# Kernel optimization log

Hardware: AMD Instinct MI355X
Metric: run time of the kernel (lower is better)

Reference implementation:

```python
import jax, jax.numpy as jnp
import numpy as np

L, B, N, W, H = 8, 8, 1024, 768, 12
C = W // H  # per-head channel dim = 64


def setup_inputs() -> dict:
    key = jax.random.key(0)
    ks = jax.random.split(key, 5)
    s = 0.02  # init scale for weights
    return {
        "x": jax.random.normal(ks[0], (B, N, W), jnp.float32),
        "Wqkv": jax.random.normal(ks[1], (L, W, 3 * W), jnp.float32) * s,
        "bqkv": jnp.zeros((L, 3 * W), jnp.float32),
        "Wo": jax.random.normal(ks[2], (L, W, W), jnp.float32) * s,
        "bo": jnp.zeros((L, W), jnp.float32),
        "Wfc": jax.random.normal(ks[3], (L, W, 4 * W), jnp.float32) * s,
        "bfc": jnp.zeros((L, 4 * W), jnp.float32),
        "Wpr": jax.random.normal(ks[4], (L, 4 * W, W), jnp.float32) * s,
        "bpr": jnp.zeros((L, W), jnp.float32),
        "g1": jnp.ones((L, W), jnp.float32),
        "b1": jnp.zeros((L, W), jnp.float32),
        "g2": jnp.ones((L, W), jnp.float32),
        "b2": jnp.zeros((L, W), jnp.float32),
    }


def _ln(x, g, b, eps=1e-5):
    m = jnp.mean(x, axis=-1, keepdims=True)
    v = jnp.var(x, axis=-1, keepdims=True)
    return (x - m) * jax.lax.rsqrt(v + eps) * g + b


def reference(x, Wqkv, bqkv, Wo, bo, Wfc, bfc, Wpr, bpr, g1, b1, g2, b2):
    scale = 1.0 / np.sqrt(np.sqrt(C))  # applied to BOTH q and k, as in source

    def block(h, p):
        wqkv, bq, wo, bo_, wfc, bf, wpr, bp, G1, B1, G2, B2 = p
        # --- attention ---
        y = _ln(h, G1, B1)
        qkv = y @ wqkv + bq                       # [B,N,3W]
        qkv = qkv.reshape(B, N, H, 3 * C)         # per-head interleaved q|k|v
        q, k, v = jnp.split(qkv, 3, axis=-1)      # each [B,N,H,C]
        w = jnp.einsum('bthc,bshc->bhts', q * scale, k * scale)
        w = jax.nn.softmax(w.astype(jnp.float32), axis=-1).astype(w.dtype)
        attn = jnp.einsum('bhts,bshc->bthc', w, v).reshape(B, N, W)
        h = h + attn @ wo + bo_
        # --- MLP (exact GELU, matching torch F.gelu default) ---
        y2 = _ln(h, G2, B2)
        h = h + jax.nn.gelu(y2 @ wfc + bf, approximate=False) @ wpr + bp
        return h, None

    out, _ = jax.lax.scan(block, x, (Wqkv, bqkv, Wo, bo, Wfc, bfc, Wpr, bpr, g1, b1, g2, b2))
    return out
```

## Files before the change

kernel.cpp:

```cpp
#include <hip/hip_runtime.h>
#include <hip/hip_bf16.h>
#include <cstdint>
#include <cstddef>


typedef __attribute__((ext_vector_type(8))) short bf16x8;
typedef __attribute__((ext_vector_type(4))) float f32x4;

#define MFMA16(a, b, c) __builtin_amdgcn_mfma_f32_16x16x32_bf16((a), (b), (c), 0, 0, 0)

__device__ __forceinline__ void gld_lds16(const void* g, void* l) {
    __builtin_amdgcn_global_load_lds((const __attribute__((address_space(1))) unsigned int*)g,
                                     (__attribute__((address_space(3))) unsigned int*)l,
                                     16, 0, 0);
}

__device__ __forceinline__ unsigned short f32_to_bf16_bits(float f) {
    unsigned u = __builtin_bit_cast(unsigned, f);
    u += 0x7fffu + ((u >> 16) & 1u);
    return (unsigned short)(u >> 16);
}

__device__ __forceinline__ unsigned pack_bf2(float a, float b) {
    return (unsigned)f32_to_bf16_bits(a) | ((unsigned)f32_to_bf16_bits(b) << 16);
}

__device__ __forceinline__ unsigned cvt_pk_bf16(float lo, float hi) {
    unsigned r;
    asm("v_cvt_pk_bf16_f32 %0, %1, %2" : "=v"(r) : "v"(lo), "v"(hi));
    return r;
}

template <bool RES, bool GELU, bool WF, bool WH>
__global__ __launch_bounds__(256) void gemm_bt(const __hip_bfloat16* __restrict__ A,
                                               const __hip_bfloat16* __restrict__ Bt,
                                               const float* __restrict__ bias,
                                               const float* __restrict__ res,
                                               float* __restrict__ outf,
                                               __hip_bfloat16* __restrict__ outh,
                                               int N, int K) {
    __shared__ __hip_bfloat16 lA0[128 * 32], lA1[128 * 32];
    __shared__ __hip_bfloat16 lB0[128 * 32], lB1[128 * 32];
    const int t = threadIdx.x;
    const int w = t >> 6, l = t & 63;
    const int lr = l & 15, lg = l >> 4;
    const int bid = blockIdx.x;
    const int xcd = bid & 7;
    const int local = bid >> 3;
    const int m0 = (xcd * 8 + (local & 7)) * 128;
    const int n0 = (local >> 3) * 128;
    const int wm = (w & 1) * 64, wn = (w >> 1) * 64;

    f32x4 acc[4][4];
#pragma unroll
    for (int i = 0; i < 4; i++)
#pragma unroll
        for (int j = 0; j < 4; j++) acc[i][j] = (f32x4){0.f, 0.f, 0.f, 0.f};

    for (int k0 = 0; k0 < K; k0 += 64) {
        __syncthreads();
#pragma unroll
        for (int i = 0; i < 2; i++) {
            int c = t + i * 256;
            int row = c >> 2, seg = c & 3;
            const size_t ab = (size_t)(m0 + row) * K + k0 + seg * 8;
            const size_t bb = (size_t)(n0 + row) * K + k0 + seg * 8;
            gld_lds16(&A[ab],       &lA0[c * 8]);
            gld_lds16(&A[ab + 32],  &lA1[c * 8]);
            gld_lds16(&Bt[bb],      &lB0[c * 8]);
            gld_lds16(&Bt[bb + 32], &lB1[c * 8]);
        }
        __syncthreads();
#pragma unroll
        for (int hh = 0; hh < 2; hh++) {
            const __hip_bfloat16* sA = hh ? lA1 : lA0;
            const __hip_bfloat16* sB = hh ? lB1 : lB0;
            bf16x8 af[4], bfr[4];
#pragma unroll
            for (int mt = 0; mt < 4; mt++)
                af[mt] = *(const bf16x8*)&sA[(wm + mt * 16 + lr) * 32 + lg * 8];
#pragma unroll
            for (int nt = 0; nt < 4; nt++)
                bfr[nt] = *(const bf16x8*)&sB[(wn + nt * 16 + lr) * 32 + lg * 8];
#pragma unroll
            for (int mt = 0; mt < 4; mt++)
#pragma unroll
                for (int nt = 0; nt < 4; nt++)
                    acc[mt][nt] = MFMA16(af[mt], bfr[nt], acc[mt][nt]);
        }
    }

#pragma unroll
    for (int nt = 0; nt < 4; nt++) {
        const int col = n0 + wn + nt * 16 + lr;
        const float bv = bias[col];
#pragma unroll
        for (int mt = 0; mt < 4; mt++) {
#pragma unroll
            for (int r = 0; r < 4; r++) {
                const int row = m0 + wm + mt * 16 + lg * 4 + r;
                const size_t idx = (size_t)row * N + col;
                float v = acc[mt][nt][r] + bv;
                if (RES) v += res[idx];
                if (GELU) v = 0.5f * v * (1.f + erff(v * 0.70710678118654752f));
                if (WF) outf[idx] = v;
                if (WH) outh[idx] = __float2bfloat16(v);
            }
        }
    }
}

__global__ __launch_bounds__(256) void ln_kernel(const float* __restrict__ h,
                                                 const float* __restrict__ g,
                                                 const float* __restrict__ b,
                                                 __hip_bfloat16* __restrict__ y) {
    const int t = threadIdx.x;
    const int w = t >> 6, l = t & 63;
    const int row = blockIdx.x * 4 + w;
    const float4* hr = (const float4*)(h + (size_t)row * 768);
    const float4* g4 = (const float4*)g;
    const float4* b4 = (const float4*)b;
    float4 x[3];
    float s = 0.f, q = 0.f;
#pragma unroll
    for (int j = 0; j < 3; j++) {
        x[j] = hr[l + j * 64];
        s += x[j].x + x[j].y + x[j].z + x[j].w;
        q += x[j].x * x[j].x + x[j].y * x[j].y + x[j].z * x[j].z + x[j].w * x[j].w;
    }
#pragma unroll
    for (int d = 1; d < 64; d <<= 1) {
        s += __shfl_xor(s, d);
        q += __shfl_xor(q, d);
    }
    const float mean = s * (1.f / 768.f);
    const float var = q * (1.f / 768.f) - mean * mean;
    const float rs = rsqrtf(var + 1e-5f);
    uint2* yr = (uint2*)(y + (size_t)row * 768);
#pragma unroll
    for (int j = 0; j < 3; j++) {
        const float4 gg = g4[l + j * 64], bb = b4[l + j * 64];
        float o0 = (x[j].x - mean) * rs * gg.x + bb.x;
        float o1 = (x[j].y - mean) * rs * gg.y + bb.y;
        float o2 = (x[j].z - mean) * rs * gg.z + bb.z;
        float o3 = (x[j].w - mean) * rs * gg.w + bb.w;
        yr[l + j * 64] = make_uint2(pack_bf2(o0, o1), pack_bf2(o2, o3));
    }
}

__global__ __launch_bounds__(256) void transpose_weights(const float* __restrict__ sq,
                                                         const float* __restrict__ so,
                                                         const float* __restrict__ sf,
                                                         const float* __restrict__ sp,
                                                         __hip_bfloat16* __restrict__ dq,
                                                         __hip_bfloat16* __restrict__ dO,
                                                         __hip_bfloat16* __restrict__ df,
                                                         __hip_bfloat16* __restrict__ dp) {
    const int bid = blockIdx.x;
    const float* src;
    __hip_bfloat16* dst;
    int K, N, tloc;
    if (bid < 1728)      { src = sq; dst = dq; K = 768;  N = 2304; tloc = bid; }
    else if (bid < 2304) { src = so; dst = dO; K = 768;  N = 768;  tloc = bid - 1728; }
    else if (bid < 4608) { src = sf; dst = df; K = 768;  N = 3072; tloc = bid - 2304; }
    else                 { src = sp; dst = dp; K = 3072; N = 768;  tloc = bid - 4608; }
    const int ktiles = K / 32;
    const int k0 = (tloc % ktiles) * 32;
    const int n0 = (tloc / ktiles) * 32;
    const int t = threadIdx.x;
    __shared__ float tile[32][33];
#pragma unroll
    for (int p = 0; p < 4; p++) {
        int rr = p * 8 + (t >> 5);
        tile[rr][t & 31] = src[(size_t)(k0 + rr) * N + n0 + (t & 31)];
    }
    __syncthreads();
#pragma unroll
    for (int p = 0; p < 4; p++) {
        int rr = p * 8 + (t >> 5);
        dst[(size_t)(n0 + rr) * K + k0 + (t & 31)] = __float2bfloat16(tile[t & 31][rr]);
    }
}

__global__ __launch_bounds__(256) void vt_transpose(const short* __restrict__ qkv,
                                                    short* __restrict__ vt) {
    const int bid = blockIdx.x;
    const int bh = bid >> 6, tau = bid & 63;
    const int b = bh / 12, h = bh % 12;
    const int ct = tau >> 5, nt = tau & 31;
    const int n0 = nt * 32, c0 = ct * 32;
    const int t = threadIdx.x;
    __shared__ short tile[32][33];
    const short* base = qkv + (size_t)(b * 1024 + n0) * 2304 + h * 192 + 128 + c0;
#pragma unroll
    for (int p = 0; p < 4; p++) {
        int rr = p * 8 + (t >> 5);
        tile[rr][t & 31] = base[(size_t)rr * 2304 + (t & 31)];
    }
    __syncthreads();
    short* ob = vt + (size_t)((b * 12 + h) * 64 + c0) * 1024 + n0;
#pragma unroll
    for (int p = 0; p < 4; p++) {
        int rr = p * 8 + (t >> 5);
        ob[(size_t)rr * 1024 + (t & 31)] = tile[t & 31][rr];
    }
}

__global__ __launch_bounds__(256) void attn_kernel(const short* __restrict__ qkv,
                                                   const short* __restrict__ vt,
                                                   short* __restrict__ attnout) {
    const int bid = blockIdx.x;
    const int xcd = bid & 7, j = bid >> 3;
    const int bh = xcd * 12 + (j >> 4);
    const int qt = j & 15;
    const int b = bh / 12, hh = bh % 12;
    const int t = threadIdx.x, w = t >> 6, l = t & 63;
    const int lr = l & 15, lg = l >> 4;
    const int x7 = lr & 7;
    __shared__ short lK[64 * 64];
    __shared__ short lV[64 * 64];
    __shared__ short lP[4][16 * 64];
    const int qw = qt * 64 + w * 16;

    bf16x8 bq[2];
#pragma unroll
    for (int ks = 0; ks < 2; ks++)
        bq[ks] = *(const bf16x8*)&qkv[(size_t)(b * 1024 + qw + lr) * 2304 + hh * 192 + ks * 32 + lg * 8];

    int col[2];
    col[0] = (lg ^ x7) * 8;
    col[1] = ((4 | lg) ^ x7) * 8;

    const int c0 = t, c1 = t + 256;
    const int r0 = c0 >> 3, r1 = c1 >> 3;
    const int s0 = (c0 & 7) ^ (r0 & 7), s1 = (c1 & 7) ^ (r1 & 7);
    const short* gK0 = qkv + (size_t)(b * 1024 + r0) * 2304 + hh * 192 + 64 + s0 * 8;
    const short* gK1 = qkv + (size_t)(b * 1024 + r1) * 2304 + hh * 192 + 64 + s1 * 8;
    const short* gV0 = vt + (size_t)((b * 12 + hh) * 64 + r0) * 1024 + s0 * 8;
    const short* gV1 = vt + (size_t)((b * 12 + hh) * 64 + r1) * 1024 + s1 * 8;

    f32x4 o[4];
#pragma unroll
    for (int dt = 0; dt < 4; dt++) o[dt] = (f32x4){0.f, 0.f, 0.f, 0.f};
    const float cexp = 0.125f * 1.44269504088896f;
    float cm = -1.0e30f;
    float lsum = 0.f;

    for (int kt = 0; kt < 16; kt++) {
        const int key0 = kt * 64;
        __syncthreads();
        gld_lds16(gK0 + (size_t)key0 * 2304, &lK[c0 * 8]);
        gld_lds16(gK1 + (size_t)key0 * 2304, &lK[c1 * 8]);
        gld_lds16(gV0 + key0, &lV[c0 * 8]);
        gld_lds16(gV1 + key0, &lV[c1 * 8]);
        __syncthreads();

        f32x4 s[4];
#pragma unroll
        for (int nt = 0; nt < 4; nt++) s[nt] = (f32x4){0.f, 0.f, 0.f, 0.f};
#pragma unroll
        for (int nt = 0; nt < 4; nt++)
#pragma unroll
            for (int ks = 0; ks < 2; ks++) {
                bf16x8 ak = *(const bf16x8*)&lK[(nt * 16 + lr) * 64 + col[ks]];
                s[nt] = MFMA16(ak, bq[ks], s[nt]);
            }

        float mx = s[0][0];
#pragma unroll
        for (int nt = 0; nt < 4; nt++)
#pragma unroll
            for (int r = 0; r < 4; r++) mx = fmaxf(mx, s[nt][r]);
        mx = fmaxf(mx, __shfl_xor(mx, 16));
        mx = fmaxf(mx, __shfl_xor(mx, 32));
        const float tm = mx * cexp;
        if (!__all(tm <= cm + 8.f)) {
            const float cmn = fmaxf(cm, tm);
            const float alpha = exp2f(cm - cmn);
            cm = cmn;
            lsum *= alpha;
            float af[4];
#pragma unroll
            for (int r = 0; r < 4; r++) af[r] = __shfl(alpha, lg * 4 + r);
#pragma unroll
            for (int dt = 0; dt < 4; dt++)
#pragma unroll
                for (int r = 0; r < 4; r++) o[dt][r] *= af[r];
        }
        float ps = 0.f;
#pragma unroll
        for (int nt = 0; nt < 4; nt++)
#pragma unroll
            for (int r = 0; r < 4; r++) {
                float p = exp2f(s[nt][r] * cexp - cm);
                s[nt][r] = p;
                ps += p;
            }
        ps += __shfl_xor(ps, 16);
        ps += __shfl_xor(ps, 32);
        lsum += ps;

#pragma unroll
        for (int nt = 0; nt < 4; nt++) {
            unsigned pk0 = cvt_pk_bf16(s[nt][0], s[nt][1]);
            unsigned pk1 = cvt_pk_bf16(s[nt][2], s[nt][3]);
            const int S = nt * 2 + (lg >> 1);
            *(uint2*)&lP[w][lr * 64 + ((S ^ x7) << 3) + ((lg & 1) << 2)] = make_uint2(pk0, pk1);
        }

#pragma unroll
        for (int kc = 0; kc < 2; kc++) {
            bf16x8 ap = *(const bf16x8*)&lP[w][lr * 64 + col[kc]];
#pragma unroll
            for (int dt = 0; dt < 4; dt++) {
                bf16x8 bv = *(const bf16x8*)&lV[(dt * 16 + lr) * 64 + col[kc]];
                o[dt] = MFMA16(ap, bv, o[dt]);
            }
        }
    }

    float inv[4];
#pragma unroll
    for (int r = 0; r < 4; r++) inv[r] = 1.f / __shfl(lsum, lg * 4 + r);
#pragma unroll
    for (int dt = 0; dt < 4; dt++)
#pragma unroll
        for (int r = 0; r < 4; r++)
            attnout[(size_t)(b * 1024 + qw + lg * 4 + r) * 768 + hh * 64 + dt * 16 + lr] =
                (short)f32_to_bf16_bits(o[dt][r] * inv[r]);
}

extern "C" void kernel_launch(void* const* d_in, const int* in_sizes, int n_in,
                              void* d_out, int out_size, void* d_ws, size_t ws_size,
                              hipStream_t stream) {
    const float* x    = (const float*)d_in[0];
    const float* Wqkv = (const float*)d_in[1];
    const float* bqkv = (const float*)d_in[2];
    const float* Wo   = (const float*)d_in[3];
    const float* bo   = (const float*)d_in[4];
    const float* Wfc  = (const float*)d_in[5];
    const float* bfc  = (const float*)d_in[6];
    const float* Wpr  = (const float*)d_in[7];
    const float* bpr  = (const float*)d_in[8];
    const float* g1   = (const float*)d_in[9];
    const float* b1   = (const float*)d_in[10];
    const float* g2   = (const float*)d_in[11];
    const float* b2   = (const float*)d_in[12];
    float* h = (float*)d_out;

    char* ws = (char*)d_ws;
    size_t off = 0;
    auto alloc = [&](size_t bytes) -> void* {
        void* p = ws + off;
        off += (bytes + 255) & ~(size_t)255;
        return p;
    };
    __hip_bfloat16* tQKV = (__hip_bfloat16*)alloc((size_t)2304 * 768 * 2);
    __hip_bfloat16* tO   = (__hip_bfloat16*)alloc((size_t)768 * 768 * 2);
    __hip_bfloat16* tFC  = (__hip_bfloat16*)alloc((size_t)3072 * 768 * 2);
    __hip_bfloat16* tPR  = (__hip_bfloat16*)alloc((size_t)768 * 3072 * 2);
    __hip_bfloat16* y    = (__hip_bfloat16*)alloc((size_t)8192 * 768 * 2);
    __hip_bfloat16* att  = (__hip_bfloat16*)alloc((size_t)8192 * 768 * 2);
    __hip_bfloat16* vtb  = (__hip_bfloat16*)alloc((size_t)8192 * 768 * 2);
    __hip_bfloat16* big  = (__hip_bfloat16*)alloc((size_t)8192 * 3072 * 2);
    __hip_bfloat16* qkvb = big;
    __hip_bfloat16* fcb  = big;

    hipMemcpyAsync(h, x, (size_t)8 * 1024 * 768 * 4, hipMemcpyDeviceToDevice, stream);

    for (int L = 0; L < 8; L++) {
        const float* wq = Wqkv + (size_t)L * 768 * 2304;
        const float* wo = Wo   + (size_t)L * 768 * 768;
        const float* wf = Wfc  + (size_t)L * 768 * 3072;
        const float* wp = Wpr  + (size_t)L * 3072 * 768;

        transpose_weights<<<6912, 256, 0, stream>>>(wq, wo, wf, wp, tQKV, tO, tFC, tPR);

        ln_kernel<<<2048, 256, 0, stream>>>(h, g1 + L * 768, b1 + L * 768, y);

        gemm_bt<false, false, false, true><<<18 * 64, 256, 0, stream>>>(
            y, tQKV, bqkv + L * 2304, nullptr, nullptr, qkvb, 2304, 768);

        vt_transpose<<<6144, 256, 0, stream>>>((const short*)qkvb, (short*)vtb);

        attn_kernel<<<1536, 256, 0, stream>>>(
            (const short*)qkvb, (const short*)vtb, (short*)att);

        gemm_bt<true, false, true, false><<<6 * 64, 256, 0, stream>>>(
            att, tO, bo + L * 768, h, h, nullptr, 768, 768);

        ln_kernel<<<2048, 256, 0, stream>>>(h, g2 + L * 768, b2 + L * 768, y);

        gemm_bt<false, true, false, true><<<24 * 64, 256, 0, stream>>>(
            y, tFC, bfc + L * 3072, nullptr, nullptr, fcb, 3072, 768);

        gemm_bt<true, false, true, false><<<6 * 64, 256, 0, stream>>>(
            fcb, tPR, bpr + L * 768, h, h, nullptr, 768, 3072);
    }
}
```

Measured before the change: 2.572 ms.

## Use 256x256-tile 512-thread GEMM with interleaved prefetch for QKV and FC

Adds a new bf16 GEMM kernel with 256x256 output tiles, 64-wide K steps, 8 waves per block and XOR-swizzled LDS. It splits each K step into four MFMA phases separated by barriers, issuing the next tile's A and B global-to-LDS loads between phases and raising wave priority around the MFMA bursts. The QKV and FC projections now use it. The larger tiles are meant to raise data reuse and hide load latency, but they use 128 KB of LDS per block and far fewer blocks, which can hurt occupancy and load balance across CUs.

```diff
diff --git a/kernel.cpp b/kernel.cpp
--- a/kernel.cpp
+++ b/kernel.cpp
@@ -29,6 +29,164 @@
     unsigned r;
     asm("v_cvt_pk_bf16_f32 %0, %1, %2" : "=v"(r) : "v"(lo), "v"(hi));
     return r;
+}
+
+template <bool GELU>
+__global__ __launch_bounds__(512, 2) void gemm256(const __hip_bfloat16* __restrict__ A,
+                                                  const __hip_bfloat16* __restrict__ Bt,
+                                                  const float* __restrict__ bias,
+                                                  __hip_bfloat16* __restrict__ outh,
+                                                  int N, int K) {
+    __shared__ __hip_bfloat16 lA[2][256 * 64];
+    __shared__ __hip_bfloat16 lB[2][256 * 64];
+    const int t = threadIdx.x;
+    const int w = t >> 6, l = t & 63;
+    const int lr = l & 15, lg = l >> 4;
+    const int wr = w >> 2, wc = w & 3;
+    const int bid = blockIdx.x;
+    const int xcd = bid & 7, local = bid >> 3;
+    const int m0 = (xcd * 4 + (local & 3)) * 256;
+    const int n0 = (local >> 2) * 256;
+
+    const int srow = t >> 3, sslot = t & 7;
+#define STAGE_A(buf, kt)                                                            \
+    {                                                                               \
+        _Pragma("unroll") for (int j = 0; j < 4; j++) {                             \
+            const int row = srow + j * 64;                                          \
+            gld_lds16(&A[(size_t)(m0 + row) * K + (kt) * 64 + ((sslot ^ (row & 7)) << 3)], \
+                      &lA[buf][(t + j * 512) * 8]);                                 \
+        }                                                                           \
+    }
+#define STAGE_B(buf, kt)                                                            \
+    {                                                                               \
+        _Pragma("unroll") for (int j = 0; j < 4; j++) {                             \
+            const int row = srow + j * 64;                                          \
+            gld_lds16(&Bt[(size_t)(n0 + row) * K + (kt) * 64 + ((sslot ^ (row & 7)) << 3)], \
+                      &lB[buf][(t + j * 512) * 8]);                                 \
+        }                                                                           \
+    }
+
+    f32x4 acc[8][4];
+#pragma unroll
+    for (int i = 0; i < 8; i++)
+#pragma unroll
+        for (int j = 0; j < 4; j++) acc[i][j] = (f32x4){0.f, 0.f, 0.f, 0.f};
+
+    STAGE_A(0, 0);
+    STAGE_B(0, 0);
+    __syncthreads();
+
+    const int NT = K >> 6;
+    for (int kt = 0; kt < NT; ++kt) {
+        const int cur = kt & 1;
+        const bool more = (kt + 1 < NT);
+        const __hip_bfloat16* sA = lA[cur];
+        const __hip_bfloat16* sB = lB[cur];
+        bf16x8 af[4][2], bf[4][2];
+
+#pragma unroll
+        for (int mt = 0; mt < 4; mt++)
+#pragma unroll
+            for (int ks = 0; ks < 2; ks++) {
+                const int row = wr * 128 + mt * 16 + lr;
+                af[mt][ks] = *(const bf16x8*)&sA[row * 64 + ((((ks << 2) | lg) ^ (row & 7)) << 3)];
+            }
+#pragma unroll
+        for (int nt = 0; nt < 2; nt++)
+#pragma unroll
+            for (int ks = 0; ks < 2; ks++) {
+                const int row = wc * 64 + nt * 16 + lr;
+                bf[nt][ks] = *(const bf16x8*)&sB[row * 64 + ((((ks << 2) | lg) ^ (row & 7)) << 3)];
+            }
+        if (more) STAGE_A(cur ^ 1, kt + 1);
+        __builtin_amdgcn_s_barrier();
+        asm volatile("s_waitcnt lgkmcnt(0)" ::: "memory");
+        __builtin_amdgcn_sched_barrier(0);
+        __builtin_amdgcn_s_setprio(1);
+#pragma unroll
+        for (int mt = 0; mt < 4; mt++)
+#pragma unroll
+            for (int nt = 0; nt < 2; nt++)
+#pragma unroll
+                for (int ks = 0; ks < 2; ks++)
+                    acc[mt][nt] = MFMA16(af[mt][ks], bf[nt][ks], acc[mt][nt]);
+        __builtin_amdgcn_s_setprio(0);
+        __builtin_amdgcn_s_barrier();
+
+#pragma unroll
+        for (int nt = 2; nt < 4; nt++)
+#pragma unroll
+            for (int ks = 0; ks < 2; ks++) {
+                const int row = wc * 64 + nt * 16 + lr;
+                bf[nt][ks] = *(const bf16x8*)&sB[row * 64 + ((((ks << 2) | lg) ^ (row & 7)) << 3)];
+            }
+        if (more) STAGE_B(cur ^ 1, kt + 1);
+        __builtin_amdgcn_s_barrier();
+        asm volatile("s_waitcnt lgkmcnt(0)" ::: "memory");
+        __builtin_amdgcn_sched_barrier(0);
+        __builtin_amdgcn_s_setprio(1);
+#pragma unroll
+        for (int mt = 0; mt < 4; mt++)
+#pragma unroll
+            for (int nt = 2; nt < 4; nt++)
+#pragma unroll
+                for (int ks = 0; ks < 2; ks++)
+                    acc[mt][nt] = MFMA16(af[mt][ks], bf[nt][ks], acc[mt][nt]);
+        __builtin_amdgcn_s_setprio(0);
+        __builtin_amdgcn_s_barrier();
+
+#pragma unroll
+        for (int mt = 0; mt < 4; mt++)
+#pragma unroll
+            for (int ks = 0; ks < 2; ks++) {
+                const int row = wr * 128 + 64 + mt * 16 + lr;
+                af[mt][ks] = *(const bf16x8*)&sA[row * 64 + ((((ks << 2) | lg) ^ (row & 7)) << 3)];
+            }
+        __builtin_amdgcn_s_barrier();
+        asm volatile("s_waitcnt lgkmcnt(0)" ::: "memory");
+        __builtin_amdgcn_sched_barrier(0);
+        __builtin_amdgcn_s_setprio(1);
+#pragma unroll
+        for (int mt = 0; mt < 4; mt++)
+#pragma unroll
+            for (int nt = 2; nt < 4; nt++)
+#pragma unroll
+                for (int ks = 0; ks < 2; ks++)
+                    acc[4 + mt][nt] = MFMA16(af[mt][ks], bf[nt][ks], acc[4 + mt][nt]);
+        __builtin_amdgcn_s_setprio(0);
+        __builtin_amdgcn_s_barrier();
+
+        __builtin_amdgcn_s_setprio(1);
+#pragma unroll
+        for (int mt = 0; mt < 4; mt++)
+#pragma unroll
+            for (int nt = 0; nt < 2; nt++)
+#pragma unroll
+                for (int ks = 0; ks < 2; ks++)
+                    acc[4 + mt][nt] = MFMA16(af[mt][ks], bf[nt][ks], acc[4 + mt][nt]);
+        __builtin_amdgcn_s_setprio(0);
+        asm volatile("s_waitcnt vmcnt(0)" ::: "memory");
+        __builtin_amdgcn_sched_barrier(0);
+        __builtin_amdgcn_s_barrier();
+    }
+#undef STAGE_A
+#undef STAGE_B
+
+#pragma unroll
+    for (int nt = 0; nt < 4; nt++) {
+        const int col = n0 + wc * 64 + nt * 16 + lr;
+        const float bv = bias[col];
+#pragma unroll
+        for (int mt = 0; mt < 8; mt++) {
+#pragma unroll
+            for (int r = 0; r < 4; r++) {
+                const int row = m0 + wr * 128 + mt * 16 + lg * 4 + r;
+                float v = acc[mt][nt][r] + bv;
+                if (GELU) v = 0.5f * v * (1.f + erff(v * 0.70710678118654752f));
+                outh[(size_t)row * N + col] = __float2bfloat16(v);
+            }
+        }
+    }
 }
 
 template <bool RES, bool GELU, bool WF, bool WH>
@@ -378,8 +536,7 @@
 
         ln_kernel<<<2048, 256, 0, stream>>>(h, g1 + L * 768, b1 + L * 768, y);
 
-        gemm_bt<false, false, false, true><<<18 * 64, 256, 0, stream>>>(
-            y, tQKV, bqkv + L * 2304, nullptr, nullptr, qkvb, 2304, 768);
+        gemm256<false><<<288, 512, 0, stream>>>(y, tQKV, bqkv + L * 2304, qkvb, 2304, 768);
 
         vt_transpose<<<6144, 256, 0, stream>>>((const short*)qkvb, (short*)vtb);
 
@@ -391,8 +548,7 @@
 
         ln_kernel<<<2048, 256, 0, stream>>>(h, g2 + L * 768, b2 + L * 768, y);
 
-        gemm_bt<false, true, false, true><<<24 * 64, 256, 0, stream>>>(
-            y, tFC, bfc + L * 3072, nullptr, nullptr, fcb, 3072, 768);
+        gemm256<true><<<384, 512, 0, stream>>>(y, tFC, bfc + L * 3072, fcb, 3072, 768);
 
         gemm_bt<true, false, true, false><<<6 * 64, 256, 0, stream>>>(
             fcb, tPR, bpr + L * 768, h, h, nullptr, 768, 3072);
```

After: 2.593 ms. No clear change (+0.8%).

## Double-buffer GEMM LDS tiles with XOR swizzle and one barrier per k-step

Applied to the files above, without the earlier changes.

Reworks the bf16 GEMM main loop so the next 64-wide K tile is prefetched into a second LDS buffer while MFMAs run on the current one. This hides global-to-LDS load latency and removes one of the two barriers per iteration. LDS rows are widened to 64 elements with an XOR swizzle on 16-byte chunks to avoid bank conflicts on fragment reads, and launch bounds request two blocks per CU. In exchange, LDS use doubles to 64 KB per block, which may limit occupancy.

```diff
diff --git a/kernel.cpp b/kernel.cpp
--- a/kernel.cpp
+++ b/kernel.cpp
@@ -32,18 +32,21 @@
 }
 
 template <bool RES, bool GELU, bool WF, bool WH>
-__global__ __launch_bounds__(256) void gemm_bt(const __hip_bfloat16* __restrict__ A,
-                                               const __hip_bfloat16* __restrict__ Bt,
-                                               const float* __restrict__ bias,
-                                               const float* __restrict__ res,
-                                               float* __restrict__ outf,
-                                               __hip_bfloat16* __restrict__ outh,
-                                               int N, int K) {
-    __shared__ __hip_bfloat16 lA0[128 * 32], lA1[128 * 32];
-    __shared__ __hip_bfloat16 lB0[128 * 32], lB1[128 * 32];
+__global__ __launch_bounds__(256, 2) void gemm_bt(const __hip_bfloat16* __restrict__ A,
+                                                  const __hip_bfloat16* __restrict__ Bt,
+                                                  const float* __restrict__ bias,
+                                                  const float* __restrict__ res,
+                                                  float* __restrict__ outf,
+                                                  __hip_bfloat16* __restrict__ outh,
+                                                  int N, int K) {
+    __shared__ __hip_bfloat16 lA[2][128 * 64];
+    __shared__ __hip_bfloat16 lB[2][128 * 64];
     const int t = threadIdx.x;
     const int w = t >> 6, l = t & 63;
     const int lr = l & 15, lg = l >> 4;
+    const int x7 = lr & 7;
+    const int cs0 = (lg ^ x7) << 3;
+    const int cs1 = ((4 | lg) ^ x7) << 3;
     const int bid = blockIdx.x;
     const int xcd = bid & 7;
     const int local = bid >> 3;
@@ -51,44 +54,57 @@
     const int n0 = (local >> 3) * 128;
     const int wm = (w & 1) * 64, wn = (w >> 1) * 64;
 
+    const int srow = t >> 3, sslot = t & 7;
+    const int sx = (sslot ^ (srow & 7)) << 3;
+
     f32x4 acc[4][4];
 #pragma unroll
     for (int i = 0; i < 4; i++)
 #pragma unroll
         for (int j = 0; j < 4; j++) acc[i][j] = (f32x4){0.f, 0.f, 0.f, 0.f};
 
-    for (int k0 = 0; k0 < K; k0 += 64) {
+#define STAGE(buf, kt)                                                        \
+    {                                                                         \
+        _Pragma("unroll") for (int j = 0; j < 4; j++) {                       \
+            const int row = srow + j * 32;                                    \
+            const int gcol = (kt) * 64 + sx;                                  \
+            gld_lds16(&A[(size_t)(m0 + row) * K + gcol], &lA[buf][(t + j * 256) * 8]); \
+            gld_lds16(&Bt[(size_t)(n0 + row) * K + gcol], &lB[buf][(t + j * 256) * 8]); \
+        }                                                                     \
+    }
+
+    STAGE(0, 0);
+    __syncthreads();
+
+    const int NT = K >> 6;
+    for (int kt = 0; kt < NT; ++kt) {
+        const int cur = kt & 1;
+        if (kt + 1 < NT) STAGE(cur ^ 1, kt + 1);
+        const __hip_bfloat16* sA = lA[cur];
+        const __hip_bfloat16* sB = lB[cur];
+        bf16x8 af[4][2], bf[4][2];
+#pragma unroll
+        for (int mt = 0; mt < 4; mt++) {
+            const int ro = (wm + mt * 16 + lr) * 64;
+            af[mt][0] = *(const bf16x8*)&sA[ro + cs0];
+            af[mt][1] = *(const bf16x8*)&sA[ro + cs1];
+        }
+#pragma unroll
+        for (int nt = 0; nt < 4; nt++) {
+            const int ro = (wn + nt * 16 + lr) * 64;
+            bf[nt][0] = *(const bf16x8*)&sB[ro + cs0];
+            bf[nt][1] = *(const bf16x8*)&sB[ro + cs1];
+        }
+#pragma unroll
+        for (int mt = 0; mt < 4; mt++)
+#pragma unroll
+            for (int nt = 0; nt < 4; nt++) {
+                acc[mt][nt] = MFMA16(af[mt][0], bf[nt][0], acc[mt][nt]);
+                acc[mt][nt] = MFMA16(af[mt][1], bf[nt][1], acc[mt][nt]);
+            }
         __syncthreads();
-#pragma unroll
-        for (int i = 0; i < 2; i++) {
-            int c = t + i * 256;
-            int row = c >> 2, seg = c & 3;
-            const size_t ab = (size_t)(m0 + row) * K + k0 + seg * 8;
-            const size_t bb = (size_t)(n0 + row) * K + k0 + seg * 8;
-            gld_lds16(&A[ab],       &lA0[c * 8]);
-            gld_lds16(&A[ab + 32],  &lA1[c * 8]);
-            gld_lds16(&Bt[bb],      &lB0[c * 8]);
-            gld_lds16(&Bt[bb + 32], &lB1[c * 8]);
-        }
-        __syncthreads();
-#pragma unroll
-        for (int hh = 0; hh < 2; hh++) {
-            const __hip_bfloat16* sA = hh ? lA1 : lA0;
-            const __hip_bfloat16* sB = hh ? lB1 : lB0;
-            bf16x8 af[4], bfr[4];
-#pragma unroll
-            for (int mt = 0; mt < 4; mt++)
-                af[mt] = *(const bf16x8*)&sA[(wm + mt * 16 + lr) * 32 + lg * 8];
-#pragma unroll
-            for (int nt = 0; nt < 4; nt++)
-                bfr[nt] = *(const bf16x8*)&sB[(wn + nt * 16 + lr) * 32 + lg * 8];
-#pragma unroll
-            for (int mt = 0; mt < 4; mt++)
-#pragma unroll
-                for (int nt = 0; nt < 4; nt++)
-                    acc[mt][nt] = MFMA16(af[mt], bfr[nt], acc[mt][nt]);
-        }
-    }
+    }
+#undef STAGE
 
 #pragma unroll
     for (int nt = 0; nt < 4; nt++) {
```

New measurement: 2.391 ms. -7.0%, faster.
